# Kernel tuning notes

Hardware: AMD Instinct MI355X
Metric: run time of the kernel (lower is better)

## Reference

```python
import jax, jax.numpy as jnp
import numpy as np

B, S, E = 2, 2048, 1024
H, HD = 16, 64
ROPE, NOPE = 32, 32          # qk_rope_head_dim, head_dim - rope
QL, KVL = 512, 512           # q_lora_rank, kv_lora_rank
EPS = 1e-5


def _layernorm(u, g, b):
    mu = jnp.mean(u, axis=-1, keepdims=True)
    var = jnp.mean(jnp.square(u - mu), axis=-1, keepdims=True)
    return (u - mu) * jax.lax.rsqrt(var + EPS) * g + b


def _rope_tables(seq_len):
    inv_freq = 1.0 / (10000.0 ** (jnp.arange(0, ROPE, 2, dtype=jnp.float32) / ROPE))
    freqs = jnp.arange(seq_len, dtype=jnp.float32)[:, None] * inv_freq[None, :]  # [S, ROPE/2]
    return jnp.cos(freqs), jnp.sin(freqs)


def _apply_rope(t, cos, sin):
    # t: [B, H, S, ROPE]; cos/sin: [S, ROPE/2]
    x1, x2 = t[..., ::2], t[..., 1::2]
    c = cos[None, None, :, :]
    s = sin[None, None, :, :]
    r1 = x1 * c - x2 * s
    r2 = x1 * s + x2 * c
    return jnp.stack([r1, r2], axis=-1).reshape(t.shape)  # interleave back


def setup_inputs() -> dict:
    key = jax.random.key(0)
    ks = jax.random.split(key, 8)
    w = 0.02
    return {
        "x": jax.random.normal(ks[0], (B, S, E), dtype=jnp.float32),
        "Wqa": jax.random.normal(ks[1], (QL, E), dtype=jnp.float32) * w,
        "g_qa": jnp.ones((QL,), jnp.float32),
        "b_qa": jnp.zeros((QL,), jnp.float32),
        "Wqb": jax.random.normal(ks[2], (H * HD, QL), dtype=jnp.float32) * w,
        "Wkva": jax.random.normal(ks[3], (KVL + ROPE, E), dtype=jnp.float32) * w,
        "g_kva": jnp.ones((KVL,), jnp.float32),
        "b_kva": jnp.zeros((KVL,), jnp.float32),
        "Wkvb": jax.random.normal(ks[4], (H * (NOPE + HD), KVL), dtype=jnp.float32) * w,
        "Wout": jax.random.normal(ks[5], (E, H * HD), dtype=jnp.float32) * w,
    }


def reference(x, Wqa, g_qa, b_qa, Wqb, Wkva, g_kva, b_kva, Wkvb, Wout):
    # --- query path: low-rank compress -> LN -> decompress ---
    qc = _layernorm(jnp.einsum('bse,re->bsr', x, Wqa), g_qa, b_qa)      # [B,S,QL]
    q = jnp.einsum('bsr,dr->bsd', qc, Wqb).reshape(B, S, H, HD)
    q = q.transpose(0, 2, 1, 3)                                          # [B,H,S,HD]
    q_nope, q_pe = q[..., :NOPE], q[..., NOPE:]

    # --- kv path: joint compress with decoupled rope part ---
    kva = jnp.einsum('bse,re->bsr', x, Wkva)                             # [B,S,KVL+ROPE]
    ckv, k_pe = kva[..., :KVL], kva[..., KVL:]
    ckv = _layernorm(ckv, g_kva, b_kva)
    kvd = jnp.einsum('bsr,dr->bsd', ckv, Wkvb).reshape(B, S, H, NOPE + HD)
    kvd = kvd.transpose(0, 2, 1, 3)                                       # [B,H,S,NOPE+HD]
    k_nope, v = kvd[..., :NOPE], kvd[..., NOPE:]
    k_pe = k_pe[:, None, :, :]                                            # [B,1,S,ROPE]

    # --- decoupled RoPE ---
    cos, sin = _rope_tables(S)
    q_pe = _apply_rope(q_pe, cos, sin)
    k_pe = jnp.broadcast_to(_apply_rope(k_pe, cos, sin), (B, H, S, ROPE))

    q_full = jnp.concatenate([q_nope, q_pe], axis=-1)                     # [B,H,S,HD]
    k_full = jnp.concatenate([k_nope, k_pe], axis=-1)

    scale = 1.0 / np.sqrt(HD).astype(np.float32)
    scores = jnp.einsum('bhsd,bhtd->bhst', q_full, k_full) * scale        # [B,H,S,S]
    attn = jax.nn.softmax(scores, axis=-1)
    out = jnp.einsum('bhst,bhtd->bhsd', attn, v)                          # [B,H,S,HD]
    out = out.transpose(0, 2, 1, 3).reshape(B, S, H * HD)
    return jnp.einsum('bsd,ed->bse', out, Wout)
```

## Files before the change

### kernel.cpp

```cpp
#include <hip/hip_runtime.h>
#include <math.h>

#define B_SZ 2
#define S_SZ 2048
#define E_SZ 1024
#define H_SZ 16
#define HD_SZ 64

#define ATT_SCALE 0.1803368801111306f
#define ROPE_L2 0.8304820237218407f

typedef unsigned short u16;
typedef unsigned int u32;
typedef __bf16 bf16_t;
typedef bf16_t bf16x8 __attribute__((ext_vector_type(8)));
typedef float f32x4 __attribute__((ext_vector_type(4)));

__device__ __forceinline__ u16 f2bf(float f) {
    bf16_t h = (bf16_t)f;
    union { bf16_t h; u16 u; } v; v.h = h;
    return v.u;
}
__device__ __forceinline__ float bf2f(u16 u) {
    union { u32 u; float f; } v; v.u = ((u32)u) << 16; return v.f;
}

__device__ __forceinline__ void gload_lds16(const void* g, void* l) {
    __builtin_amdgcn_global_load_lds(
        (const __attribute__((address_space(1))) unsigned int*)g,
        (__attribute__((address_space(3))) unsigned int*)l, 16, 0, 0);
}

#define N_X   4194304L
#define N_QA  524288L
#define N_QB  524288L
#define N_KVA 557056L
#define N_KVB 786432L

__global__ __launch_bounds__(256) void init_kernel(
    const float* __restrict__ x, const float* __restrict__ wqa,
    const float* __restrict__ wqb, const float* __restrict__ wkva,
    const float* __restrict__ wkvb, const float* __restrict__ wout,
    u16* __restrict__ xb, u16* __restrict__ wqab, u16* __restrict__ wqbb,
    u16* __restrict__ wkvab, u16* __restrict__ wkvbb, u16* __restrict__ woutb,
    float2* __restrict__ tbl)
{
    if (blockIdx.x < 128) {
        const int idx = blockIdx.x * 256 + threadIdx.x;
        const int s = idx >> 4, i = idx & 15;
        const float invf = exp2f(-(float)i * ROPE_L2);
        float sn, c;
        sincosf((float)s * invf, &sn, &c);
        tbl[idx] = make_float2(c, sn);
        return;
    }
    long i = ((long)(blockIdx.x - 128) * 256 + threadIdx.x) * 8;
    const long c0 = N_X, c1 = c0 + N_QA, c2 = c1 + N_QB, c3 = c2 + N_KVA, c4 = c3 + N_KVB;
    const float* src; u16* dst; long off;
    if      (i < c0) { src = x;    dst = xb;    off = i; }
    else if (i < c1) { src = wqa;  dst = wqab;  off = i - c0; }
    else if (i < c2) { src = wqb;  dst = wqbb;  off = i - c1; }
    else if (i < c3) { src = wkva; dst = wkvab; off = i - c2; }
    else if (i < c4) { src = wkvb; dst = wkvbb; off = i - c3; }
    else             { src = wout; dst = woutb; off = i - c4; }
    float v[8];
    *(float4*)v       = *(const float4*)(src + off);
    *(float4*)(v + 4) = *(const float4*)(src + off + 4);
    u32 o[4];
    #pragma unroll
    for (int k = 0; k < 4; ++k)
        o[k] = (u32)f2bf(v[2*k]) | ((u32)f2bf(v[2*k+1]) << 16);
    *(uint4*)(dst + off) = *(const uint4*)o;
}

template<bool BF16OUT>
__device__ __forceinline__ void gemm_body(
    const u16* __restrict__ A, int lda,
    const u16* __restrict__ Bm, int ldb,
    void* __restrict__ Cout, int ldc, int N, int K,
    int m0, int n0, u16* smA, u16* smB)
{
    const int tid = threadIdx.x;
    const int wave = tid >> 6, lane = tid & 63;
    const int wm = wave >> 1, wn = wave & 1;

    f32x4 acc[4][4] = {};
    const int rA0 = wm * 64 + (lane & 15);
    const int rB0 = wn * 64 + (lane & 15);
    const int cfr = lane >> 4;

    const int srow = wave * 8 + (lane >> 3);
    const int slot = lane & 7;

    for (int k0 = 0; k0 < K; k0 += 64) {
        #pragma unroll
        for (int j = 0; j < 4; ++j) {
            const int r = j * 32 + srow;
            const int boff = j * 4096 + wave * 1024 + (lane << 4);
            const int sw = (slot ^ (r & 7)) * 8;
            gload_lds16(A + (size_t)(m0 + r) * lda + k0 + sw, (char*)smA + boff);
            const int nr = min(n0 + r, N - 1);
            gload_lds16(Bm + (size_t)nr * ldb + k0 + sw, (char*)smB + boff);
        }
        __syncthreads();
        #pragma unroll
        for (int hk = 0; hk < 2; ++hk) {
            bf16x8 af[4], bfr[4];
            #pragma unroll
            for (int f = 0; f < 4; ++f) {
                const int rA = rA0 + f * 16;
                af[f]  = *(const bf16x8*)(smA + rA * 64 + (((hk * 4 + cfr) ^ (rA & 7)) * 8));
                const int rB = rB0 + f * 16;
                bfr[f] = *(const bf16x8*)(smB + rB * 64 + (((hk * 4 + cfr) ^ (rB & 7)) * 8));
            }
            #pragma unroll
            for (int i = 0; i < 4; ++i)
                #pragma unroll
                for (int j = 0; j < 4; ++j)
                    acc[i][j] = __builtin_amdgcn_mfma_f32_16x16x32_bf16(af[i], bfr[j], acc[i][j], 0, 0, 0);
        }
        __syncthreads();
    }

    const int cn = lane & 15, rq = lane >> 4;
    #pragma unroll
    for (int i = 0; i < 4; ++i) {
        #pragma unroll
        for (int j = 0; j < 4; ++j) {
            const int n = n0 + wn * 64 + j * 16 + cn;
            if (n < N) {
                #pragma unroll
                for (int r = 0; r < 4; ++r) {
                    const size_t row = (size_t)(m0 + wm * 64 + i * 16 + rq * 4 + r);
                    if (BF16OUT) ((u16*)Cout)[row * ldc + n] = f2bf(acc[i][j][r]);
                    else         ((float*)Cout)[row * ldc + n] = acc[i][j][r];
                }
            }
        }
    }
}

__device__ __forceinline__ int swz_bid() {
    const int nx = gridDim.x;
    const int bid = blockIdx.x + nx * blockIdx.y;
    const int cpx = (nx * gridDim.y) >> 3;
    return (bid & 7) * cpx + (bid >> 3);
}

template<bool BF16OUT>
__global__ __launch_bounds__(256) void gemm_bt_bf16(
    const u16* __restrict__ A, int lda,
    const u16* __restrict__ Bm, int ldb,
    void* __restrict__ Cout, int ldc, int N, int K)
{
    __shared__ u16 smA[128 * 64];
    __shared__ u16 smB[128 * 64];
    const int w = swz_bid();
    const int nx = gridDim.x;
    gemm_body<BF16OUT>(A, lda, Bm, ldb, Cout, ldc, N, K,
                       (w / nx) * 128, (w % nx) * 128, smA, smB);
}

__global__ __launch_bounds__(256) void gemm_dual(
    const u16* __restrict__ A,
    const u16* __restrict__ B1, u16* __restrict__ C1,
    const u16* __restrict__ B2, u16* __restrict__ C2)
{
    __shared__ u16 smA[128 * 64];
    __shared__ u16 smB[128 * 64];
    const int w = swz_bid();
    const int bx = w % 9, by = w / 9;
    if (bx < 4)
        gemm_body<true>(A, 1024, B1, 1024, C1, 512, 512, 1024,
                        by * 128, bx * 128, smA, smB);
    else
        gemm_body<true>(A, 1024, B2, 1024, C2, 544, 544, 1024,
                        by * 128, (bx - 4) * 128, smA, smB);
}

__global__ __launch_bounds__(256) void ln2_kernel(
    const u16* __restrict__ qc_b, const u16* __restrict__ kva_b,
    const float* __restrict__ g_qa, const float* __restrict__ b_qa,
    const float* __restrict__ g_kva, const float* __restrict__ b_kva,
    u16* __restrict__ qcb, u16* __restrict__ ckvb,
    float* __restrict__ kpe, const float2* __restrict__ tbl)
{
    const bool qpart = blockIdx.x < 4096;
    const int row = blockIdx.x & 4095;
    const u16* in      = qpart ? qc_b : kva_b;
    const int ld       = qpart ? 512 : 544;
    const float* gamma = qpart ? g_qa : g_kva;
    const float* beta  = qpart ? b_qa : b_kva;
    u16* outb          = qpart ? qcb : ckvb;

    const u16* p = in + (size_t)row * ld;
    const int t = threadIdx.x;
    const u32 w01 = *(const u32*)(p + 2 * t);
    float v0 = bf2f((u16)w01), v1 = bf2f((u16)(w01 >> 16));

    __shared__ float red[4];
    const int wave = t >> 6, lane = t & 63;

    float s = v0 + v1;
    #pragma unroll
    for (int o = 1; o < 64; o <<= 1) s += __shfl_xor(s, o);
    if (lane == 0) red[wave] = s;
    __syncthreads();
    const float mu = (red[0] + red[1] + red[2] + red[3]) * (1.f / 512.f);

    const float d0 = v0 - mu, d1 = v1 - mu;
    float s2 = d0 * d0 + d1 * d1;
    #pragma unroll
    for (int o = 1; o < 64; o <<= 1) s2 += __shfl_xor(s2, o);
    __syncthreads();
    if (lane == 0) red[wave] = s2;
    __syncthreads();
    const float var = (red[0] + red[1] + red[2] + red[3]) * (1.f / 512.f);
    const float rs = rsqrtf(var + 1e-5f);

    const float o0 = d0 * rs * gamma[2*t]     + beta[2*t];
    const float o1 = d1 * rs * gamma[2*t + 1] + beta[2*t + 1];
    *(u32*)(outb + (size_t)row * 512 + 2 * t) =
        (u32)f2bf(o0) | ((u32)f2bf(o1) << 16);

    if (!qpart && t < 16) {
        const int spos = row & (S_SZ - 1);
        const float2 cs = tbl[spos * 16 + t];
        const u32 wpe = *(const u32*)(p + 512 + 2 * t);
        const float x1 = bf2f((u16)wpe), x2 = bf2f((u16)(wpe >> 16));
        kpe[(size_t)row * 32 + 2*t]     = x1 * cs.x - x2 * cs.y;
        kpe[(size_t)row * 32 + 2*t + 1] = x1 * cs.y + x2 * cs.x;
    }
}

__global__ __launch_bounds__(256) void gemm_qkv(
    const u16* __restrict__ qcb, const u16* __restrict__ wqbb,
    const u16* __restrict__ ckvb, const u16* __restrict__ wkvbb,
    const float* __restrict__ kpe, const float2* __restrict__ tbl,
    u16* __restrict__ qpack, u16* __restrict__ kpack, u16* __restrict__ vt)
{
    __shared__ u16 smA[128 * 64];
    __shared__ u16 smB[128 * 64];
    const int tid = threadIdx.x;
    const int wsw = swz_bid();
    const int bx = wsw % 21, by = wsw / 21;

    if (bx == 20) {
        #pragma unroll
        for (int rr = 0; rr < 2; ++rr) {
            const int row = by * 128 + rr * 64 + (tid >> 2);
            const int p = 4 + (tid & 3);
            const int s = row & (S_SZ - 1), b = row >> 11;
            const float* src = kpe + (size_t)row * 32 + (p - 4) * 8;
            float v[8];
            *(float4*)v       = *(const float4*)(src);
            *(float4*)(v + 4) = *(const float4*)(src + 4);
            u32 o[4];
            #pragma unroll
            for (int k = 0; k < 4; ++k)
                o[k] = (u32)f2bf(v[2*k]) | ((u32)f2bf(v[2*k+1]) << 16);
            const int sch = p ^ (s & 7);
            #pragma unroll
            for (int h = 0; h < 16; ++h)
                *(uint4*)(kpack + (((size_t)(b * 16 + h) * S_SZ + s) * 64) + sch * 8) = *(const uint4*)o;
        }
        return;
    }

    const int wave = tid >> 6, lane = tid & 63;
    const int wm = wave >> 1, wn = wave & 1;
    const bool qpath = bx < 8;
    const u16* A  = qpath ? qcb : ckvb;
    const u16* Bm = qpath ? wqbb : wkvbb;
    const int n0 = (qpath ? bx : bx - 8) * 128;
    const int m0 = by * 128;

    f32x4 acc[4][4] = {};
    const int rA0 = wm * 64 + (lane & 15);
    const int rB0 = wn * 64 + (lane & 15);
    const int cfr = lane >> 4;
    const int srow = wave * 8 + (lane >> 3);
    const int slot = lane & 7;

    for (int k0 = 0; k0 < 512; k0 += 64) {
        #pragma unroll
        for (int j = 0; j < 4; ++j) {
            const int r = j * 32 + srow;
            const int boff = j * 4096 + wave * 1024 + (lane << 4);
            const int sw = (slot ^ (r & 7)) * 8;
            gload_lds16(A + (size_t)(m0 + r) * 512 + k0 + sw, (char*)smA + boff);
            gload_lds16(Bm + (size_t)(n0 + r) * 512 + k0 + sw, (char*)smB + boff);
        }
        __syncthreads();
        #pragma unroll
        for (int hk = 0; hk < 2; ++hk) {
            bf16x8 af[4], bfr[4];
            #pragma unroll
            for (int f = 0; f < 4; ++f) {
                const int rA = rA0 + f * 16;
                af[f]  = *(const bf16x8*)(smA + rA * 64 + (((hk * 4 + cfr) ^ (rA & 7)) * 8));
                const int rB = rB0 + f * 16;
                bfr[f] = *(const bf16x8*)(smB + rB * 64 + (((hk * 4 + cfr) ^ (rB & 7)) * 8));
            }
            #pragma unroll
            for (int i = 0; i < 4; ++i)
                #pragma unroll
                for (int j = 0; j < 4; ++j)
                    acc[i][j] = __builtin_amdgcn_mfma_f32_16x16x32_bf16(af[i], bfr[j], acc[i][j], 0, 0, 0);
        }
        __syncthreads();
    }

    const int cn = lane & 15, rq = lane >> 4;
    if (qpath) {
        #pragma unroll
        for (int i = 0; i < 4; ++i) {
            #pragma unroll
            for (int j = 0; j < 4; ++j) {
                const int n = n0 + wn * 64 + j * 16 + cn;
                const int d = n & 63, h = n >> 6;
                #pragma unroll
                for (int r = 0; r < 4; ++r) {
                    const int row = m0 + wm * 64 + i * 16 + rq * 4 + r;
                    const int s = row & (S_SZ - 1), b = row >> 11;
                    const float val = acc[i][j][r];
                    const float prt = __shfl_xor(val, 1);
                    float o;
                    if (d >= 32) {
                        const float2 cs = tbl[s * 16 + ((d - 32) >> 1)];
                        o = (d & 1) ? (prt * cs.y + val * cs.x)
                                    : (val * cs.x - prt * cs.y);
                    } else {
                        o = val;
                    }
                    o *= ATT_SCALE;
                    const int sch = (d >> 3) ^ (s & 7);
                    qpack[(((size_t)(b * 16 + h) * S_SZ + s) * 64) + sch * 8 + (d & 7)] = f2bf(o);
                }
            }
        }
    } else {
        #pragma unroll
        for (int j = 0; j < 4; ++j) {
            const int n = n0 + wn * 64 + j * 16 + cn;
            const int h = n / 96;
            const int dd = n - h * 96;
            const bool isk = dd < 32;
            const int d = dd - 32;
            #pragma unroll
            for (int i = 0; i < 4; ++i) {
                #pragma unroll
                for (int r = 0; r < 4; ++r) {
                    const int row = m0 + wm * 64 + i * 16 + rq * 4 + r;
                    const int s = row & (S_SZ - 1), b = row >> 11;
                    const u16 val = f2bf(acc[i][j][r]);
                    if (isk) {
                        kpack[(((size_t)(b * 16 + h) * S_SZ + s) * 64)
                              + (((dd >> 3) ^ (s & 7)) * 8) + (dd & 7)] = val;
                    } else {
                        const int kk = s & 63, kt = s >> 6;
                        const int jj = (kk & 32) | ((kk & 8) << 1) | ((kk & 4) << 1)
                                     | ((kk & 16) >> 2) | (kk & 3);
                        vt[(((size_t)(b * 16 + h) * 32 + kt) * 64 + d) * 64
                           + (((jj >> 3) ^ (d & 7)) * 8) + (jj & 7)] = val;
                    }
                }
            }
        }
    }
}

__global__ __launch_bounds__(256, 2) void attn_mfma_kernel(
    const u16* __restrict__ qpack, const u16* __restrict__ kpack,
    const u16* __restrict__ vt, u16* __restrict__ attout)
{
    __shared__ u16 KV[2][2][2][4096];

    const int bid = blockIdx.x;
    const int w0 = (bid & 7) * 64 + (bid >> 3);
    const int qt = w0 & 15, h = (w0 >> 4) & 15, b = w0 >> 8;
    const int bh = b * H_SZ + h;
    const int tid = threadIdx.x, wave = tid >> 6, lane = tid & 63;
    const int kw = wave >> 1, wv = wave & 1;
    const int g = lane >> 4, q15 = lane & 15;

    const u16* kbase = kpack + (size_t)bh * S_SZ * 64 + (size_t)(kw * 16) * 4096;
    const u16* vbase = vt + (size_t)bh * (S_SZ / 64) * 4096 + (size_t)(kw * 16) * 4096;

    bf16x8 qa[4][2];
    {
        const u16* qbase = qpack + ((size_t)bh * S_SZ + qt * 128) * 64;
        #pragma unroll
        for (int qb = 0; qb < 4; ++qb) {
            const int r = wv * 64 + qb * 16 + q15;
            #pragma unroll
            for (int dh = 0; dh < 2; ++dh) {
                const int ch = dh * 4 + g;
                qa[qb][dh] = *(const bf16x8*)(qbase + r * 64 + ((ch ^ (r & 7)) * 8));
            }
        }
    }

    int koff[4][2], voff[2][4];
    #pragma unroll
    for (int fk = 0; fk < 4; ++fk) {
        const int kc = fk * 16 + q15;
        #pragma unroll
        for (int dh = 0; dh < 2; ++dh)
            koff[fk][dh] = kc * 128 + (((dh * 4 + g) ^ (kc & 7)) * 16);
    }
    #pragma unroll
    for (int kh = 0; kh < 2; ++kh)
        #pragma unroll
        for (int fd = 0; fd < 4; ++fd) {
            const int d = fd * 16 + q15;
            voff[kh][fd] = 8192 + d * 128 + (((kh * 4 + g) ^ (d & 7)) * 16);
        }

    #pragma unroll
    for (int j = 0; j < 4; ++j) {
        const int boff = j * 2048 + wv * 1024;
        gload_lds16(kbase + boff / 2 + lane * 8, (char*)&KV[kw][0][0][0] + boff);
        gload_lds16(vbase + boff / 2 + lane * 8, (char*)&KV[kw][0][1][0] + boff);
    }
    __syncthreads();

    bf16x8 ones;
    #pragma unroll
    for (int e = 0; e < 8; ++e) ones[e] = (bf16_t)1.0f;

    f32x4 acc[4][4] = {};
    f32x4 acc_l[4] = {};

    #pragma unroll 2
    for (int t = 0; t < 16; ++t) {
        const char* base = (const char*)&KV[kw][t & 1][0][0];
        char* nbase = (char*)&KV[kw][(t + 1) & 1][0][0];

        if (t != 15) {
            const u16* kn = kbase + (size_t)(t + 1) * 4096;
            const u16* vn = vbase + (size_t)(t + 1) * 4096;
            #pragma unroll
            for (int j = 0; j < 4; ++j) {
                const int boff = j * 2048 + wv * 1024;
                gload_lds16(kn + boff / 2 + lane * 8, nbase + boff);
                gload_lds16(vn + boff / 2 + lane * 8, nbase + 8192 + boff);
            }
        }

        bf16x8 kb[4][2];
        #pragma unroll
        for (int fk = 0; fk < 4; ++fk)
            #pragma unroll
            for (int dh = 0; dh < 2; ++dh)
                kb[fk][dh] = *(const bf16x8*)(base + koff[fk][dh]);

        f32x4 sc[4][4] = {};
        __builtin_amdgcn_s_setprio(1);
        #pragma unroll
        for (int qb = 0; qb < 4; ++qb)
            #pragma unroll
            for (int fk = 0; fk < 4; ++fk)
                #pragma unroll
                for (int dh = 0; dh < 2; ++dh)
                    sc[qb][fk] = __builtin_amdgcn_mfma_f32_16x16x32_bf16(kb[fk][dh], qa[qb][dh], sc[qb][fk], 0, 0, 0);
        __builtin_amdgcn_s_setprio(0);

        #pragma unroll
        for (int qb = 0; qb < 4; ++qb)
            #pragma unroll
            for (int fk = 0; fk < 4; ++fk)
                #pragma unroll
                for (int r = 0; r < 4; ++r)
                    sc[qb][fk][r] = __builtin_amdgcn_exp2f(sc[qb][fk][r]);

        bf16x8 pa[4][2];
        #pragma unroll
        for (int qb = 0; qb < 4; ++qb)
            #pragma unroll
            for (int kh = 0; kh < 2; ++kh)
                #pragma unroll
                for (int e = 0; e < 4; ++e) {
                    pa[qb][kh][e]     = (bf16_t)sc[qb][2*kh][e];
                    pa[qb][kh][e + 4] = (bf16_t)sc[qb][2*kh + 1][e];
                }

        bf16x8 vb[2][4];
        #pragma unroll
        for (int kh = 0; kh < 2; ++kh)
            #pragma unroll
            for (int fd = 0; fd < 4; ++fd)
                vb[kh][fd] = *(const bf16x8*)(base + voff[kh][fd]);

        __builtin_amdgcn_s_setprio(1);
        #pragma unroll
        for (int kh = 0; kh < 2; ++kh)
            #pragma unroll
            for (int qb = 0; qb < 4; ++qb) {
                #pragma unroll
                for (int fd = 0; fd < 4; ++fd)
                    acc[qb][fd] = __builtin_amdgcn_mfma_f32_16x16x32_bf16(vb[kh][fd], pa[qb][kh], acc[qb][fd], 0, 0, 0);
                acc_l[qb] = __builtin_amdgcn_mfma_f32_16x16x32_bf16(ones, pa[qb][kh], acc_l[qb], 0, 0, 0);
            }
        __builtin_amdgcn_s_setprio(0);

        __syncthreads();
    }

    float* ex = (float*)&KV[0][0][0][0];
    const int slot = (wv * 64 + lane) * 68;
    if (kw == 1) {
        #pragma unroll
        for (int qb = 0; qb < 4; ++qb)
            #pragma unroll
            for (int fd = 0; fd < 4; ++fd)
                *(f32x4*)(ex + slot + (qb * 4 + fd) * 4) = acc[qb][fd];
        #pragma unroll
        for (int qb = 0; qb < 4; ++qb)
            ex[slot + 64 + qb] = acc_l[qb][0];
    }
    __syncthreads();
    if (kw == 0) {
        #pragma unroll
        for (int qb = 0; qb < 4; ++qb) {
            const float l2 = acc_l[qb][0] + ex[slot + 64 + qb];
            const float inv = 1.0f / l2;
            const size_t row = (size_t)(b * S_SZ + qt * 128 + wv * 64 + qb * 16 + q15);
            #pragma unroll
            for (int fd = 0; fd < 4; ++fd) {
                const f32x4 o = acc[qb][fd] + *(const f32x4*)(ex + slot + (qb * 4 + fd) * 4);
                const int d0 = fd * 16 + 4 * g;
                u32 wlo = (u32)f2bf(o[0] * inv) | ((u32)f2bf(o[1] * inv) << 16);
                u32 whi = (u32)f2bf(o[2] * inv) | ((u32)f2bf(o[3] * inv) << 16);
                *(uint2*)(attout + row * 1024 + h * 64 + d0) = make_uint2(wlo, whi);
            }
        }
    }
}

extern "C" void kernel_launch(void* const* d_in, const int* in_sizes, int n_in,
                              void* d_out, int out_size, void* d_ws, size_t ws_size,
                              hipStream_t stream)
{
    (void)in_sizes; (void)n_in; (void)out_size; (void)ws_size;
    const float* x     = (const float*)d_in[0];
    const float* Wqa   = (const float*)d_in[1];
    const float* g_qa  = (const float*)d_in[2];
    const float* b_qa  = (const float*)d_in[3];
    const float* Wqb   = (const float*)d_in[4];
    const float* Wkva  = (const float*)d_in[5];
    const float* g_kva = (const float*)d_in[6];
    const float* b_kva = (const float*)d_in[7];
    const float* Wkvb  = (const float*)d_in[8];
    const float* Wout  = (const float*)d_in[9];
    float* out = (float*)d_out;

    u16* p = (u16*)d_ws;
    u16* xb     = p;
    u16* qpack  = p;  p += 4194304;
    u16* attout = p;  p += 4194304;
    u16* qc_b   = p;  p += 2097152;
    u16* kva_b  = p;  p += 2228224;
    u16* qcb    = p;  p += 2097152;
    u16* ckvb   = p;  p += 2097152;
    u16* kpack  = p;  p += 4194304;
    u16* vt     = p;  p += 4194304;
    float* kpe  = (float*)p;  p += 262144;
    float2* tbl = (float2*)p; p += 131072;
    u16* wqab   = p;  p += 524288;
    u16* wqbb   = p;  p += 524288;
    u16* wkvab  = p;  p += 557056;
    u16* wkvbb  = p;  p += 786432;
    u16* woutb  = p;  p += 1048576;

    dim3 blk(256);

    init_kernel<<<3856, blk, 0, stream>>>(x, Wqa, Wqb, Wkva, Wkvb, Wout,
                                          xb, wqab, wqbb, wkvab, wkvbb, woutb, tbl);
    gemm_dual<<<dim3(9, 32), blk, 0, stream>>>(xb, wqab, qc_b, wkvab, kva_b);
    ln2_kernel<<<8192, blk, 0, stream>>>(qc_b, kva_b, g_qa, b_qa, g_kva, b_kva,
                                         qcb, ckvb, kpe, tbl);
    gemm_qkv<<<dim3(21, 32), blk, 0, stream>>>(qcb, wqbb, ckvb, wkvbb, kpe, tbl,
                                               qpack, kpack, vt);
    attn_mfma_kernel<<<dim3(512), dim3(256), 0, stream>>>(qpack, kpack, vt, attout);
    gemm_bt_bf16<false><<<dim3(8, 32), blk, 0, stream>>>(attout, 1024, woutb, 1024, out, 1024, 1024, 1024);
}
```

Before: 127.9 us.

## Load K/V fragments straight from global into registers, dropping LDS staging

The attention kernel no longer stages K and V tiles in shared memory with async copies and barriers. Each wave now loads its own K/V MFMA fragments directly from global memory into registers, double-buffered across two tile sets. Each wave owns 64 query rows over the full key range, so the split-K reduction through LDS goes away, and the grid halves to 256 blocks of 256 query rows. The cost is that the four waves each fetch the same K/V data separately, which relies on L2/cache hits, and register pressure rises under launch_bounds(256,1).

```diff
diff --git a/kernel.cpp b/kernel.cpp
--- a/kernel.cpp
+++ b/kernel.cpp
@@ -370,60 +370,104 @@
     }
 }
 
-__global__ __launch_bounds__(256, 2) void attn_mfma_kernel(
+__device__ __forceinline__ void load_kt(const u16* __restrict__ p,
+                                        bf16x8 (&kb)[4][2], int q15, int g)
+{
+    #pragma unroll
+    for (int fk = 0; fk < 4; ++fk) {
+        const int kc = fk * 16 + q15;
+        #pragma unroll
+        for (int dh = 0; dh < 2; ++dh)
+            kb[fk][dh] = *(const bf16x8*)(p + kc * 64 + (((dh * 4 + g) ^ (kc & 7)) * 8));
+    }
+}
+__device__ __forceinline__ void load_vt(const u16* __restrict__ p,
+                                        bf16x8 (&vb)[2][4], int q15, int g)
+{
+    #pragma unroll
+    for (int kh = 0; kh < 2; ++kh)
+        #pragma unroll
+        for (int fd = 0; fd < 4; ++fd) {
+            const int d = fd * 16 + q15;
+            vb[kh][fd] = *(const bf16x8*)(p + d * 64 + (((kh * 4 + g) ^ (d & 7)) * 8));
+        }
+}
+
+__device__ __forceinline__ void attn_tile_compute(
+    const bf16x8 (&kb)[4][2], const bf16x8 (&vb)[2][4],
+    const bf16x8 (&qa)[4][2], const bf16x8 ones,
+    f32x4 (&acc)[4][4], f32x4 (&acc_l)[4])
+{
+    f32x4 sc[4][4] = {};
+    __builtin_amdgcn_s_setprio(1);
+    #pragma unroll
+    for (int qb = 0; qb < 4; ++qb)
+        #pragma unroll
+        for (int fk = 0; fk < 4; ++fk)
+            #pragma unroll
+            for (int dh = 0; dh < 2; ++dh)
+                sc[qb][fk] = __builtin_amdgcn_mfma_f32_16x16x32_bf16(kb[fk][dh], qa[qb][dh], sc[qb][fk], 0, 0, 0);
+    __builtin_amdgcn_s_setprio(0);
+
+    #pragma unroll
+    for (int qb = 0; qb < 4; ++qb)
+        #pragma unroll
+        for (int fk = 0; fk < 4; ++fk)
+            #pragma unroll
+            for (int r = 0; r < 4; ++r)
+                sc[qb][fk][r] = __builtin_amdgcn_exp2f(sc[qb][fk][r]);
+
+    bf16x8 pa[4][2];
+    #pragma unroll
+    for (int qb = 0; qb < 4; ++qb)
+        #pragma unroll
+        for (int kh = 0; kh < 2; ++kh)
+            #pragma unroll
+            for (int e = 0; e < 4; ++e) {
+                pa[qb][kh][e]     = (bf16_t)sc[qb][2*kh][e];
+                pa[qb][kh][e + 4] = (bf16_t)sc[qb][2*kh + 1][e];
+            }
+
+    __builtin_amdgcn_s_setprio(1);
+    #pragma unroll
+    for (int kh = 0; kh < 2; ++kh)
+        #pragma unroll
+        for (int qb = 0; qb < 4; ++qb) {
+            #pragma unroll
+            for (int fd = 0; fd < 4; ++fd)
+                acc[qb][fd] = __builtin_amdgcn_mfma_f32_16x16x32_bf16(vb[kh][fd], pa[qb][kh], acc[qb][fd], 0, 0, 0);
+            acc_l[qb] = __builtin_amdgcn_mfma_f32_16x16x32_bf16(ones, pa[qb][kh], acc_l[qb], 0, 0, 0);
+        }
+    __builtin_amdgcn_s_setprio(0);
+}
+
+__global__ __launch_bounds__(256, 1) void attn_mfma_kernel(
     const u16* __restrict__ qpack, const u16* __restrict__ kpack,
     const u16* __restrict__ vt, u16* __restrict__ attout)
 {
-    __shared__ u16 KV[2][2][2][4096];
-
     const int bid = blockIdx.x;
-    const int w0 = (bid & 7) * 64 + (bid >> 3);
-    const int qt = w0 & 15, h = (w0 >> 4) & 15, b = w0 >> 8;
+    const int w0 = (bid & 7) * 32 + (bid >> 3);
+    const int qt = w0 & 7, h = (w0 >> 3) & 15, b = w0 >> 7;
     const int bh = b * H_SZ + h;
     const int tid = threadIdx.x, wave = tid >> 6, lane = tid & 63;
-    const int kw = wave >> 1, wv = wave & 1;
     const int g = lane >> 4, q15 = lane & 15;
 
-    const u16* kbase = kpack + (size_t)bh * S_SZ * 64 + (size_t)(kw * 16) * 4096;
-    const u16* vbase = vt + (size_t)bh * (S_SZ / 64) * 4096 + (size_t)(kw * 16) * 4096;
+    const u16* kbase = kpack + (size_t)bh * S_SZ * 64;
+    const u16* vbase = vt + (size_t)bh * (S_SZ / 64) * 4096;
 
     bf16x8 qa[4][2];
     {
-        const u16* qbase = qpack + ((size_t)bh * S_SZ + qt * 128) * 64;
+        const u16* qbase = qpack + ((size_t)bh * S_SZ + qt * 256 + wave * 64) * 64;
         #pragma unroll
         for (int qb = 0; qb < 4; ++qb) {
-            const int r = wv * 64 + qb * 16 + q15;
+            const int r = qb * 16 + q15;
             #pragma unroll
             for (int dh = 0; dh < 2; ++dh) {
                 const int ch = dh * 4 + g;
-                qa[qb][dh] = *(const bf16x8*)(qbase + r * 64 + ((ch ^ (r & 7)) * 8));
-            }
-        }
-    }
-
-    int koff[4][2], voff[2][4];
-    #pragma unroll
-    for (int fk = 0; fk < 4; ++fk) {
-        const int kc = fk * 16 + q15;
-        #pragma unroll
-        for (int dh = 0; dh < 2; ++dh)
-            koff[fk][dh] = kc * 128 + (((dh * 4 + g) ^ (kc & 7)) * 16);
-    }
-    #pragma unroll
-    for (int kh = 0; kh < 2; ++kh)
-        #pragma unroll
-        for (int fd = 0; fd < 4; ++fd) {
-            const int d = fd * 16 + q15;
-            voff[kh][fd] = 8192 + d * 128 + (((kh * 4 + g) ^ (d & 7)) * 16);
-        }
-
-    #pragma unroll
-    for (int j = 0; j < 4; ++j) {
-        const int boff = j * 2048 + wv * 1024;
-        gload_lds16(kbase + boff / 2 + lane * 8, (char*)&KV[kw][0][0][0] + boff);
-        gload_lds16(vbase + boff / 2 + lane * 8, (char*)&KV[kw][0][1][0] + boff);
-    }
-    __syncthreads();
+                qa[qb][dh] = *(const bf16x8*)(qbase + r * 64 + ((ch ^ (q15 & 7)) * 8));
+            }
+        }
+    }
 
     bf16x8 ones;
     #pragma unroll
@@ -432,108 +476,31 @@
     f32x4 acc[4][4] = {};
     f32x4 acc_l[4] = {};
 
-    #pragma unroll 2
-    for (int t = 0; t < 16; ++t) {
-        const char* base = (const char*)&KV[kw][t & 1][0][0];
-        char* nbase = (char*)&KV[kw][(t + 1) & 1][0][0];
-
-        if (t != 15) {
-            const u16* kn = kbase + (size_t)(t + 1) * 4096;
-            const u16* vn = vbase + (size_t)(t + 1) * 4096;
-            #pragma unroll
-            for (int j = 0; j < 4; ++j) {
-                const int boff = j * 2048 + wv * 1024;
-                gload_lds16(kn + boff / 2 + lane * 8, nbase + boff);
-                gload_lds16(vn + boff / 2 + lane * 8, nbase + 8192 + boff);
-            }
-        }
-
-        bf16x8 kb[4][2];
-        #pragma unroll
-        for (int fk = 0; fk < 4; ++fk)
-            #pragma unroll
-            for (int dh = 0; dh < 2; ++dh)
-                kb[fk][dh] = *(const bf16x8*)(base + koff[fk][dh]);
-
-        f32x4 sc[4][4] = {};
-        __builtin_amdgcn_s_setprio(1);
-        #pragma unroll
-        for (int qb = 0; qb < 4; ++qb)
-            #pragma unroll
-            for (int fk = 0; fk < 4; ++fk)
-                #pragma unroll
-                for (int dh = 0; dh < 2; ++dh)
-                    sc[qb][fk] = __builtin_amdgcn_mfma_f32_16x16x32_bf16(kb[fk][dh], qa[qb][dh], sc[qb][fk], 0, 0, 0);
-        __builtin_amdgcn_s_setprio(0);
-
-        #pragma unroll
-        for (int qb = 0; qb < 4; ++qb)
-            #pragma unroll
-            for (int fk = 0; fk < 4; ++fk)
-                #pragma unroll
-                for (int r = 0; r < 4; ++r)
-                    sc[qb][fk][r] = __builtin_amdgcn_exp2f(sc[qb][fk][r]);
-
-        bf16x8 pa[4][2];
-        #pragma unroll
-        for (int qb = 0; qb < 4; ++qb)
-            #pragma unroll
-            for (int kh = 0; kh < 2; ++kh)
-                #pragma unroll
-                for (int e = 0; e < 4; ++e) {
-                    pa[qb][kh][e]     = (bf16_t)sc[qb][2*kh][e];
-                    pa[qb][kh][e + 4] = (bf16_t)sc[qb][2*kh + 1][e];
-                }
-
-        bf16x8 vb[2][4];
-        #pragma unroll
-        for (int kh = 0; kh < 2; ++kh)
-            #pragma unroll
-            for (int fd = 0; fd < 4; ++fd)
-                vb[kh][fd] = *(const bf16x8*)(base + voff[kh][fd]);
-
-        __builtin_amdgcn_s_setprio(1);
-        #pragma unroll
-        for (int kh = 0; kh < 2; ++kh)
-            #pragma unroll
-            for (int qb = 0; qb < 4; ++qb) {
-                #pragma unroll
-                for (int fd = 0; fd < 4; ++fd)
-                    acc[qb][fd] = __builtin_amdgcn_mfma_f32_16x16x32_bf16(vb[kh][fd], pa[qb][kh], acc[qb][fd], 0, 0, 0);
-                acc_l[qb] = __builtin_amdgcn_mfma_f32_16x16x32_bf16(ones, pa[qb][kh], acc_l[qb], 0, 0, 0);
-            }
-        __builtin_amdgcn_s_setprio(0);
-
-        __syncthreads();
-    }
-
-    float* ex = (float*)&KV[0][0][0][0];
-    const int slot = (wv * 64 + lane) * 68;
-    if (kw == 1) {
-        #pragma unroll
-        for (int qb = 0; qb < 4; ++qb)
-            #pragma unroll
-            for (int fd = 0; fd < 4; ++fd)
-                *(f32x4*)(ex + slot + (qb * 4 + fd) * 4) = acc[qb][fd];
-        #pragma unroll
-        for (int qb = 0; qb < 4; ++qb)
-            ex[slot + 64 + qb] = acc_l[qb][0];
-    }
-    __syncthreads();
-    if (kw == 0) {
-        #pragma unroll
-        for (int qb = 0; qb < 4; ++qb) {
-            const float l2 = acc_l[qb][0] + ex[slot + 64 + qb];
-            const float inv = 1.0f / l2;
-            const size_t row = (size_t)(b * S_SZ + qt * 128 + wv * 64 + qb * 16 + q15);
-            #pragma unroll
-            for (int fd = 0; fd < 4; ++fd) {
-                const f32x4 o = acc[qb][fd] + *(const f32x4*)(ex + slot + (qb * 4 + fd) * 4);
-                const int d0 = fd * 16 + 4 * g;
-                u32 wlo = (u32)f2bf(o[0] * inv) | ((u32)f2bf(o[1] * inv) << 16);
-                u32 whi = (u32)f2bf(o[2] * inv) | ((u32)f2bf(o[3] * inv) << 16);
-                *(uint2*)(attout + row * 1024 + h * 64 + d0) = make_uint2(wlo, whi);
-            }
+    bf16x8 kA[4][2], vA[2][4], kB[4][2], vB[2][4];
+    load_kt(kbase, kA, q15, g);
+    load_vt(vbase, vA, q15, g);
+
+    for (int t = 0; t < 32; t += 2) {
+        load_kt(kbase + (size_t)(t + 1) * 4096, kB, q15, g);
+        load_vt(vbase + (size_t)(t + 1) * 4096, vB, q15, g);
+        attn_tile_compute(kA, vA, qa, ones, acc, acc_l);
+        if (t + 2 < 32) {
+            load_kt(kbase + (size_t)(t + 2) * 4096, kA, q15, g);
+            load_vt(vbase + (size_t)(t + 2) * 4096, vA, q15, g);
+        }
+        attn_tile_compute(kB, vB, qa, ones, acc, acc_l);
+    }
+
+    #pragma unroll
+    for (int qb = 0; qb < 4; ++qb) {
+        const float inv = 1.0f / acc_l[qb][0];
+        const size_t row = (size_t)(b * S_SZ + qt * 256 + wave * 64 + qb * 16 + q15);
+        #pragma unroll
+        for (int fd = 0; fd < 4; ++fd) {
+            const int d0 = fd * 16 + 4 * g;
+            u32 wlo = (u32)f2bf(acc[qb][fd][0] * inv) | ((u32)f2bf(acc[qb][fd][1] * inv) << 16);
+            u32 whi = (u32)f2bf(acc[qb][fd][2] * inv) | ((u32)f2bf(acc[qb][fd][3] * inv) << 16);
+            *(uint2*)(attout + row * 1024 + h * 64 + d0) = make_uint2(wlo, whi);
         }
     }
 }
@@ -582,6 +549,6 @@
                                          qcb, ckvb, kpe, tbl);
     gemm_qkv<<<dim3(21, 32), blk, 0, stream>>>(qcb, wqbb, ckvb, wkvbb, kpe, tbl,
                                                qpack, kpack, vt);
-    attn_mfma_kernel<<<dim3(512), dim3(256), 0, stream>>>(qpack, kpack, vt, attout);
+    attn_mfma_kernel<<<dim3(256), dim3(256), 0, stream>>>(qpack, kpack, vt, attout);
     gemm_bt_bf16<false><<<dim3(8, 32), blk, 0, stream>>>(attout, 1024, woutb, 1024, out, 1024, 1024, 1024);
 }
```

Result: slower. 142.7 us (+11.6%).
